# Optimization experiments

Measured on AMD Instinct MI355X. Metric: run time of the kernel, lower is better.

The kernel has to match this reference:

```python
import jax, jax.numpy as jnp
import numpy as np

N_USER = 100000
N_ITEM = 100000
N_EDGE = 1600000
IN_U = 128
IN_I = 128
OUT = 64
NEG_SLOPE = 0.01  # torch F.leaky_relu default


def setup_inputs() -> dict:
    key = jax.random.key(0)
    ks = jax.random.split(key, 12)
    return {
        'feat_user': jax.random.normal(ks[0], (N_USER, IN_U), jnp.float32),
        'feat_item': jax.random.normal(ks[1], (N_ITEM, IN_I), jnp.float32),
        'W_user': jax.random.normal(ks[2], (IN_U, OUT), jnp.float32) * 0.05,
        'b_user': jax.random.normal(ks[3], (OUT,), jnp.float32) * 0.05,
        'W_item': jax.random.normal(ks[4], (IN_I, OUT), jnp.float32) * 0.05,
        'b_item': jax.random.normal(ks[5], (OUT,), jnp.float32) * 0.05,
        'attn_w': jax.random.normal(ks[6], (2 * OUT, 1), jnp.float32) * 0.05,
        'src_u2i': jax.random.randint(ks[7], (N_EDGE,), 0, N_USER),
        'dst_u2i': jax.random.randint(ks[8], (N_EDGE,), 0, N_ITEM),
        'src_i2u': jax.random.randint(ks[9], (N_EDGE,), 0, N_ITEM),
        'dst_i2u': jax.random.randint(ks[10], (N_EDGE,), 0, N_USER),
    }


def _segment_softmax(e, seg, num_segments):
    # e: [E], seg: [E] destination ids -> softmax over edges sharing a dst
    m = jax.ops.segment_max(e, seg, num_segments=num_segments)
    ex = jnp.exp(e - m[seg])
    s = jax.ops.segment_sum(ex, seg, num_segments=num_segments)
    return ex / s[seg]


def _etype_aggregate(Wh_src, Wh_dst, attn_w, src, dst, n_dst):
    # gather per-edge src/dst projected features: [E, OUT]
    zs = Wh_src[src]
    zd = Wh_dst[dst]
    # attn([zs || zd]) == zs @ a_src + zd @ a_dst (split the 2*OUT weight)
    a_src, a_dst = attn_w[:OUT, 0], attn_w[OUT:, 0]
    e = zs @ a_src + zd @ a_dst  # [E]
    e = jnp.where(e > 0, e, NEG_SLOPE * e)  # leaky_relu
    alpha = _segment_softmax(e, dst, n_dst)  # [E]
    # weighted scatter-sum into destination nodes
    return jax.ops.segment_sum(alpha[:, None] * zs, dst, num_segments=n_dst)


def reference(feat_user, feat_item, W_user, b_user, W_item, b_item, attn_w,
              src_u2i, dst_u2i, src_i2u, dst_i2u):
    Wh_user = feat_user @ W_user + b_user  # fc['user'] (etype 'user': user->item)
    Wh_item = feat_item @ W_item + b_item  # fc['item'] (etype 'item': item->user)
    # etype 'user': user -> item; dst attention feature is Wh_item on item nodes
    h_item = _etype_aggregate(Wh_user, Wh_item, attn_w, src_u2i, dst_u2i, N_ITEM)
    # etype 'item': item -> user
    h_user = _etype_aggregate(Wh_item, Wh_user, attn_w, src_i2u, dst_i2u, N_USER)
    # update_nodes sums all 'self_*' per ntype; each ntype has exactly one here
    return jnp.concatenate([h_user, h_item], axis=0)  # [N_USER+N_ITEM, OUT]
```

## Files before the change

### kernel.cpp

```cpp
#include <hip/hip_runtime.h>
#include <hip/hip_bf16.h>

#define NU 100000
#define NI 100000
#define NE 1600000
#define KIN 128
#define KOUT 64

#define NCOPY 8
#define PBK 128
#define NP 782
#define CAP2 384
#define CHUNK 4096
#define SRTSZ (NCOPY * CAP2 + PBK * 3)
#define AGG_THREADS 512
#define NWAVE 8

__device__ __forceinline__ unsigned short f2bf(float f) {
    unsigned u = __float_as_uint(f);
    unsigned r = (u + 0x7fffu + ((u >> 16) & 1u)) >> 16;
    return (unsigned short)r;
}
__device__ __forceinline__ float bf2f(unsigned short h) {
    return __uint_as_float(((unsigned)h) << 16);
}

__global__ __launch_bounds__(256) void linear_attn_kernel(
    const float* __restrict__ A0, const float* __restrict__ W0, const float* __restrict__ bv0,
    const float* __restrict__ A1, const float* __restrict__ W1, const float* __restrict__ bv1,
    const float* __restrict__ attn,
    unsigned short* __restrict__ Wh0, float* __restrict__ su0, float* __restrict__ sd0,
    unsigned short* __restrict__ Wh1, float* __restrict__ su1, float* __restrict__ sd1)
{
    __shared__ float4 Wl[128 * 16];
    __shared__ float  Al[16 * 132];
    __shared__ float  bl[64];
    __shared__ float  asrc[64], adst[64];

    int half = gridDim.x >> 1;
    bool second = blockIdx.x >= (unsigned)half;
    const float* A = second ? A1 : A0;
    const float* W = second ? W1 : W0;
    const float* bvec = second ? bv1 : bv0;
    unsigned short* Wh = second ? Wh1 : Wh0;
    float* s_src = second ? su1 : su0;
    float* s_dst = second ? sd1 : sd0;
    int blk = second ? (blockIdx.x - half) : blockIdx.x;

    int t = threadIdx.x;
    for (int i = t; i < 128 * 16; i += 256) Wl[i] = ((const float4*)W)[i];
    if (t < 64) { bl[t] = bvec[t]; asrc[t] = attn[t]; adst[t] = attn[64 + t]; }
    __syncthreads();

    int r  = t >> 4;
    int k4 = t & 15;
    int nChunks = NU / 16;
    for (int c = blk; c < nChunks; c += half) {
        const float4* Ag = (const float4*)(A + (size_t)c * 16 * 128);
        __syncthreads();
        for (int i = t; i < 512; i += 256) {
            float4 v = Ag[i];
            int rr = i >> 5;
            int cc = (i & 31) * 4;
            float* dp = &Al[rr * 132 + cc];
            dp[0] = v.x; dp[1] = v.y; dp[2] = v.z; dp[3] = v.w;
        }
        __syncthreads();

        float4 acc = {0.f, 0.f, 0.f, 0.f};
        const float* arow = &Al[r * 132];
        #pragma unroll 8
        for (int kk = 0; kk < 128; kk++) {
            float a = arow[kk];
            float4 w = Wl[kk * 16 + k4];
            acc.x += a * w.x; acc.y += a * w.y; acc.z += a * w.z; acc.w += a * w.w;
        }
        acc.x += bl[k4 * 4 + 0]; acc.y += bl[k4 * 4 + 1];
        acc.z += bl[k4 * 4 + 2]; acc.w += bl[k4 * 4 + 3];

        int row = c * 16 + r;
        ushort4 o;
        o.x = f2bf(acc.x); o.y = f2bf(acc.y); o.z = f2bf(acc.z); o.w = f2bf(acc.w);
        ((ushort4*)(Wh + (size_t)row * KOUT))[k4] = o;

        float p1 = acc.x * asrc[k4*4] + acc.y * asrc[k4*4+1] + acc.z * asrc[k4*4+2] + acc.w * asrc[k4*4+3];
        float p2 = acc.x * adst[k4*4] + acc.y * adst[k4*4+1] + acc.z * adst[k4*4+2] + acc.w * adst[k4*4+3];
        #pragma unroll
        for (int off = 8; off; off >>= 1) {
            p1 += __shfl_down(p1, off);
            p2 += __shfl_down(p2, off);
        }
        if (k4 == 0) { s_src[row] = p1; s_dst[row] = p2; }
    }
}

__global__ __launch_bounds__(256) void scatter_kernel(
    const int* __restrict__ src_u2i, const int* __restrict__ dst_u2i,
    const int* __restrict__ src_i2u, const int* __restrict__ dst_i2u,
    int* __restrict__ cur_item, int* __restrict__ cur_user,
    int* __restrict__ ebuf_item, int* __restrict__ ebuf_user,
    int nE, int nbs)
{
    __shared__ int raw[CHUNK];
    __shared__ unsigned short bkt[CHUNK];
    __shared__ int cnt[NP];
    __shared__ int gbase[NP];
    __shared__ int lcur[NP];

    bool u2i = blockIdx.x < (unsigned)nbs;
    int blk = u2i ? blockIdx.x : (blockIdx.x - nbs);
    int copy = blockIdx.x & (NCOPY - 1);
    const int* src = u2i ? src_u2i : src_i2u;
    const int* dst = u2i ? dst_u2i : dst_i2u;
    int* cur  = (u2i ? cur_item : cur_user) + copy * NP;
    int* ebuf = (u2i ? ebuf_item : ebuf_user) + (size_t)copy * NP * CAP2;

    int t = threadIdx.x;
    for (int i = t; i < NP; i += 256) { cnt[i] = 0; lcur[i] = 0; }
    __syncthreads();

    int e0 = blk * CHUNK;
    int n = nE - e0; if (n > CHUNK) n = CHUNK;

    for (int j = t; j < n; j += 256) {
        int s = src[e0 + j], d = dst[e0 + j];
        int b = d >> 7;
        raw[j] = s | ((d & 127) << 17);
        bkt[j] = (unsigned short)b;
        atomicAdd(&cnt[b], 1);
    }
    __syncthreads();

    for (int b = t; b < NP; b += 256) {
        int c = cnt[b];
        if (c) gbase[b] = atomicAdd(&cur[b], c);
    }
    __syncthreads();

    for (int j = t; j < n; j += 256) {
        int b = bkt[j];
        int p = gbase[b] + atomicAdd(&lcur[b], 1);
        if (p < CAP2) ebuf[(size_t)b * CAP2 + p] = raw[j];
    }
}

__global__ __launch_bounds__(AGG_THREADS) void agg_kernel(
    const int* __restrict__ cur_item, const int* __restrict__ cur_user,
    const int* __restrict__ ebuf_item, const int* __restrict__ ebuf_user,
    const float* __restrict__ su_user, const float* __restrict__ sd_item,
    const float* __restrict__ su_item, const float* __restrict__ sd_user,
    const unsigned short* __restrict__ Wh_user, const unsigned short* __restrict__ Wh_item,
    float* __restrict__ h_item, float* __restrict__ h_user)
{
    __shared__ int   raw[SRTSZ];
    __shared__ int   srt[SRTSZ];
    __shared__ int   offs[NCOPY + 1];
    __shared__ int   cnt[PBK];
    __shared__ int   base[PBK + 1];
    __shared__ int   cursor[PBK];
    __shared__ float sdl[PBK];

    int bid = blockIdx.x;
    bool item_side = bid < NP;
    int b = item_side ? bid : bid - NP;
    const int*   cur  = item_side ? cur_item : cur_user;
    const int*   ebuf = item_side ? ebuf_item : ebuf_user;
    const float* ssrc = item_side ? su_user : su_item;
    const float* sdst = item_side ? sd_item : sd_user;
    const unsigned short* Whs = item_side ? Wh_user : Wh_item;
    float* h = item_side ? h_item : h_user;

    int t = threadIdx.x;
    if (t < PBK) {
        cnt[t] = 0;
        int node = b * PBK + t;
        sdl[t] = (node < NU) ? sdst[node] : 0.f;
    }
    if (t == 0) {
        int a = 0;
        #pragma unroll
        for (int c = 0; c < NCOPY; c++) {
            offs[c] = a;
            int cc = cur[c * NP + b];
            if (cc > CAP2) cc = CAP2;
            a += cc;
        }
        offs[NCOPY] = a;
    }
    for (int j = t; j < SRTSZ; j += AGG_THREADS) srt[j] = 0;
    __syncthreads();

    int total = offs[NCOPY];

    for (int j = t; j < total; j += AGG_THREADS) {
        int c = 0;
        while (j >= offs[c + 1]) c++;
        int e = ebuf[((size_t)c * NP + b) * CAP2 + (j - offs[c])];
        raw[j] = e;
        atomicAdd(&cnt[e >> 17], 1);
    }
    __syncthreads();

    if (t == 0) {
        int a = 0;
        for (int i = 0; i < PBK; i++) {
            base[i] = a; cursor[i] = a;
            a += (cnt[i] + 3) & ~3;
        }
        base[PBK] = a;
    }
    __syncthreads();

    for (int j = t; j < total; j += AGG_THREADS) {
        int e = raw[j];
        int p = atomicAdd(&cursor[e >> 17], 1);
        srt[p] = e;
    }
    __syncthreads();

    int lane = t & 63;
    int wv = t >> 6;

    float* wgt = (float*)raw;
    for (int dl = wv; dl < PBK; dl += NWAVE) {
        int jb = base[dl], cc = cnt[dl], pc = base[dl + 1] - jb;
        float sd = sdl[dl];
        for (int k = lane; k < pc; k += 64) {
            float w = 0.f;
            if (k < cc) {
                int s = srt[jb + k] & 0x1FFFF;
                float ev = ssrc[s] + sd;
                ev = ev > 0.f ? ev : 0.01f * ev;
                w = __expf(ev);
            }
            wgt[jb + k] = w;
        }
    }
    __syncthreads();

    int sub = lane >> 4;
    int ch4 = (lane & 15) << 2;
    const unsigned short* WhCh = Whs + ch4;
    for (int dl = wv; dl < PBK; dl += NWAVE) {
        int node = b * PBK + dl;
        if (node >= NU) break;
        int jb = base[dl];
        int pc = base[dl + 1] - jb;
        int cc = cnt[dl];
        float ax = 0.f, ay = 0.f, az = 0.f, aw = 0.f, ssum = 0.f;
        for (int q = 0; q < pc; q += 4) {
            int j = jb + q + sub;
            int e = srt[j];
            float w = wgt[j];
            int s = e & 0x1FFFF;
            uint2 u = *(const uint2*)(WhCh + ((size_t)s << 6));
            float f0 = __uint_as_float(u.x << 16);
            float f1 = __uint_as_float(u.x & 0xffff0000u);
            float f2 = __uint_as_float(u.y << 16);
            float f3 = __uint_as_float(u.y & 0xffff0000u);
            ax += w * f0; ay += w * f1; az += w * f2; aw += w * f3;
            ssum += w;
        }
        #pragma unroll
        for (int off = 16; off <= 32; off <<= 1) {
            ax += __shfl_xor(ax, off);
            ay += __shfl_xor(ay, off);
            az += __shfl_xor(az, off);
            aw += __shfl_xor(aw, off);
            ssum += __shfl_xor(ssum, off);
        }
        if (sub == 0) {
            float inv = (cc > 0) ? 1.f / ssum : 0.f;
            float4 o = {ax * inv, ay * inv, az * inv, aw * inv};
            *(float4*)(h + (size_t)node * KOUT + ch4) = o;
        }
    }
}

extern "C" void kernel_launch(void* const* d_in, const int* in_sizes, int n_in,
                              void* d_out, int out_size, void* d_ws, size_t ws_size,
                              hipStream_t stream)
{
    const float* feat_user = (const float*)d_in[0];
    const float* feat_item = (const float*)d_in[1];
    const float* W_user    = (const float*)d_in[2];
    const float* b_user    = (const float*)d_in[3];
    const float* W_item    = (const float*)d_in[4];
    const float* b_item    = (const float*)d_in[5];
    const float* attn_w    = (const float*)d_in[6];
    const int*   src_u2i   = (const int*)d_in[7];
    const int*   dst_u2i   = (const int*)d_in[8];
    const int*   src_i2u   = (const int*)d_in[9];
    const int*   dst_i2u   = (const int*)d_in[10];

    float* out    = (float*)d_out;
    float* h_user = out;
    float* h_item = out + (size_t)NU * KOUT;

    char* p = (char*)d_ws;
    unsigned short* Wh_user = (unsigned short*)p; p += (size_t)NU * KOUT * 2;
    unsigned short* Wh_item = (unsigned short*)p; p += (size_t)NI * KOUT * 2;
    float* su_user = (float*)p; p += NU * 4;
    float* sd_user = (float*)p; p += NU * 4;
    float* su_item = (float*)p; p += NI * 4;
    float* sd_item = (float*)p; p += NI * 4;
    int* cur_item  = (int*)p; p += (size_t)NCOPY * NP * 4;
    int* cur_user  = (int*)p; p += (size_t)NCOPY * NP * 4;
    int* ebuf_item = (int*)p; p += (size_t)NCOPY * NP * CAP2 * 4;
    int* ebuf_user = (int*)p; p += (size_t)NCOPY * NP * CAP2 * 4;

    hipMemsetAsync(cur_item, 0, (size_t)2 * NCOPY * NP * 4, stream);

    int nbs = (NE + CHUNK - 1) / CHUNK;
    scatter_kernel<<<2 * nbs, 256, 0, stream>>>(src_u2i, dst_u2i, src_i2u, dst_i2u,
                                                cur_item, cur_user, ebuf_item, ebuf_user,
                                                NE, nbs);
    linear_attn_kernel<<<4096, 256, 0, stream>>>(feat_user, W_user, b_user,
                                                 feat_item, W_item, b_item, attn_w,
                                                 Wh_user, su_user, sd_user,
                                                 Wh_item, su_item, sd_item);
    agg_kernel<<<2 * NP, AGG_THREADS, 0, stream>>>(cur_item, cur_user, ebuf_item, ebuf_user,
                                                   su_user, sd_item, su_item, sd_user,
                                                   Wh_user, Wh_item, h_item, h_user);
}
```

Before: 356.2 us.

## Register-tile the projection GEMM and locally sort edges before global scatter

The linear projection kernel now gives each thread a 4x4 output micro-tile over a 64-row shared tile, using float4 loads of A and W, with a smaller persistent grid. This raises arithmetic intensity per shared-memory read. The scatter kernel now counting-sorts each chunk by destination bucket in shared memory before writing to global buffers, so writes to each bucket are contiguous. In exchange it uses more shared memory and adds an extra prefix-scan pass and barrier.

```diff
diff --git a/kernel.cpp b/kernel.cpp
--- a/kernel.cpp
+++ b/kernel.cpp
@@ -16,6 +16,10 @@
 #define AGG_THREADS 512
 #define NWAVE 8
 
+#define LIN_ROWS 64
+#define LIN_GRID 512
+#define LIN_ITERS 1563
+
 __device__ __forceinline__ unsigned short f2bf(float f) {
     unsigned u = __float_as_uint(f);
     unsigned r = (u + 0x7fffu + ((u >> 16) & 1u)) >> 16;
@@ -32,10 +36,8 @@
     unsigned short* __restrict__ Wh0, float* __restrict__ su0, float* __restrict__ sd0,
     unsigned short* __restrict__ Wh1, float* __restrict__ su1, float* __restrict__ sd1)
 {
-    __shared__ float4 Wl[128 * 16];
-    __shared__ float  Al[16 * 132];
-    __shared__ float  bl[64];
-    __shared__ float  asrc[64], adst[64];
+    __shared__ float Wl[128 * 64];
+    __shared__ float Al[LIN_ROWS * 132];
 
     int half = gridDim.x >> 1;
     bool second = blockIdx.x >= (unsigned)half;
@@ -48,49 +50,78 @@
     int blk = second ? (blockIdx.x - half) : blockIdx.x;
 
     int t = threadIdx.x;
-    for (int i = t; i < 128 * 16; i += 256) Wl[i] = ((const float4*)W)[i];
-    if (t < 64) { bl[t] = bvec[t]; asrc[t] = attn[t]; adst[t] = attn[64 + t]; }
-    __syncthreads();
-
-    int r  = t >> 4;
-    int k4 = t & 15;
-    int nChunks = NU / 16;
-    for (int c = blk; c < nChunks; c += half) {
-        const float4* Ag = (const float4*)(A + (size_t)c * 16 * 128);
+    int c4 = t & 15;
+    int rt = t >> 4;
+
+    for (int i = t; i < 128 * 64 / 4; i += 256) ((float4*)Wl)[i] = ((const float4*)W)[i];
+
+    float4 bias4 = *(const float4*)(bvec + c4 * 4);
+    float4 as4   = *(const float4*)(attn + c4 * 4);
+    float4 ad4   = *(const float4*)(attn + 64 + c4 * 4);
+
+    for (int c = blk; c < LIN_ITERS; c += half) {
+        int rowbase = c * LIN_ROWS;
         __syncthreads();
-        for (int i = t; i < 512; i += 256) {
-            float4 v = Ag[i];
-            int rr = i >> 5;
-            int cc = (i & 31) * 4;
-            float* dp = &Al[rr * 132 + cc];
-            dp[0] = v.x; dp[1] = v.y; dp[2] = v.z; dp[3] = v.w;
+        for (int g = t; g < LIN_ROWS * 32; g += 256) {
+            int rr = g >> 5;
+            int q  = g & 31;
+            float4 v = {0.f, 0.f, 0.f, 0.f};
+            int grow = rowbase + rr;
+            if (grow < NU) v = ((const float4*)(A + (size_t)grow * 128))[q];
+            *(float4*)&Al[rr * 132 + q * 4] = v;
         }
         __syncthreads();
 
-        float4 acc = {0.f, 0.f, 0.f, 0.f};
-        const float* arow = &Al[r * 132];
-        #pragma unroll 8
-        for (int kk = 0; kk < 128; kk++) {
-            float a = arow[kk];
-            float4 w = Wl[kk * 16 + k4];
-            acc.x += a * w.x; acc.y += a * w.y; acc.z += a * w.z; acc.w += a * w.w;
-        }
-        acc.x += bl[k4 * 4 + 0]; acc.y += bl[k4 * 4 + 1];
-        acc.z += bl[k4 * 4 + 2]; acc.w += bl[k4 * 4 + 3];
-
-        int row = c * 16 + r;
-        ushort4 o;
-        o.x = f2bf(acc.x); o.y = f2bf(acc.y); o.z = f2bf(acc.z); o.w = f2bf(acc.w);
-        ((ushort4*)(Wh + (size_t)row * KOUT))[k4] = o;
-
-        float p1 = acc.x * asrc[k4*4] + acc.y * asrc[k4*4+1] + acc.z * asrc[k4*4+2] + acc.w * asrc[k4*4+3];
-        float p2 = acc.x * adst[k4*4] + acc.y * adst[k4*4+1] + acc.z * adst[k4*4+2] + acc.w * adst[k4*4+3];
+        float4 acc0 = bias4, acc1 = bias4, acc2 = bias4, acc3 = bias4;
+        const float* Ar = &Al[(rt * 4) * 132];
+        const float* Wc = &Wl[c4 * 4];
+        #pragma unroll 4
+        for (int kq = 0; kq < 128; kq += 4) {
+            float4 a0 = *(const float4*)&Ar[0 * 132 + kq];
+            float4 a1 = *(const float4*)&Ar[1 * 132 + kq];
+            float4 a2 = *(const float4*)&Ar[2 * 132 + kq];
+            float4 a3 = *(const float4*)&Ar[3 * 132 + kq];
+            float4 w0 = *(const float4*)&Wc[(kq + 0) * 64];
+            float4 w1 = *(const float4*)&Wc[(kq + 1) * 64];
+            float4 w2 = *(const float4*)&Wc[(kq + 2) * 64];
+            float4 w3 = *(const float4*)&Wc[(kq + 3) * 64];
+            acc0.x += a0.x*w0.x + a0.y*w1.x + a0.z*w2.x + a0.w*w3.x;
+            acc0.y += a0.x*w0.y + a0.y*w1.y + a0.z*w2.y + a0.w*w3.y;
+            acc0.z += a0.x*w0.z + a0.y*w1.z + a0.z*w2.z + a0.w*w3.z;
+            acc0.w += a0.x*w0.w + a0.y*w1.w + a0.z*w2.w + a0.w*w3.w;
+            acc1.x += a1.x*w0.x + a1.y*w1.x + a1.z*w2.x + a1.w*w3.x;
+            acc1.y += a1.x*w0.y + a1.y*w1.y + a1.z*w2.y + a1.w*w3.y;
+            acc1.z += a1.x*w0.z + a1.y*w1.z + a1.z*w2.z + a1.w*w3.z;
+            acc1.w += a1.x*w0.w + a1.y*w1.w + a1.z*w2.w + a1.w*w3.w;
+            acc2.x += a2.x*w0.x + a2.y*w1.x + a2.z*w2.x + a2.w*w3.x;
+            acc2.y += a2.x*w0.y + a2.y*w1.y + a2.z*w2.y + a2.w*w3.y;
+            acc2.z += a2.x*w0.z + a2.y*w1.z + a2.z*w2.z + a2.w*w3.z;
+            acc2.w += a2.x*w0.w + a2.y*w1.w + a2.z*w2.w + a2.w*w3.w;
+            acc3.x += a3.x*w0.x + a3.y*w1.x + a3.z*w2.x + a3.w*w3.x;
+            acc3.y += a3.x*w0.y + a3.y*w1.y + a3.z*w2.y + a3.w*w3.y;
+            acc3.z += a3.x*w0.z + a3.y*w1.z + a3.z*w2.z + a3.w*w3.z;
+            acc3.w += a3.x*w0.w + a3.y*w1.w + a3.z*w2.w + a3.w*w3.w;
+        }
+
+        float4 accs[4] = {acc0, acc1, acc2, acc3};
         #pragma unroll
-        for (int off = 8; off; off >>= 1) {
-            p1 += __shfl_down(p1, off);
-            p2 += __shfl_down(p2, off);
-        }
-        if (k4 == 0) { s_src[row] = p1; s_dst[row] = p2; }
+        for (int i = 0; i < 4; i++) {
+            int row = rowbase + rt * 4 + i;
+            float4 av = accs[i];
+            if (row < NU) {
+                ushort4 o;
+                o.x = f2bf(av.x); o.y = f2bf(av.y); o.z = f2bf(av.z); o.w = f2bf(av.w);
+                ((ushort4*)(Wh + (size_t)row * KOUT))[c4] = o;
+            }
+            float p1 = av.x*as4.x + av.y*as4.y + av.z*as4.z + av.w*as4.w;
+            float p2 = av.x*ad4.x + av.y*ad4.y + av.z*ad4.z + av.w*ad4.w;
+            #pragma unroll
+            for (int off = 8; off; off >>= 1) {
+                p1 += __shfl_down(p1, off, 16);
+                p2 += __shfl_down(p2, off, 16);
+            }
+            if (c4 == 0 && row < NU) { s_src[row] = p1; s_dst[row] = p2; }
+        }
     }
 }
 
@@ -103,9 +134,12 @@
 {
     __shared__ int raw[CHUNK];
     __shared__ unsigned short bkt[CHUNK];
+    __shared__ int srt_[CHUNK];
+    __shared__ unsigned short sbk[CHUNK];
     __shared__ int cnt[NP];
-    __shared__ int gbase[NP];
-    __shared__ int lcur[NP];
+    __shared__ int gb[NP];
+    __shared__ int pb[NP];
+    __shared__ int lc[NP];
 
     bool u2i = blockIdx.x < (unsigned)nbs;
     int blk = u2i ? blockIdx.x : (blockIdx.x - nbs);
@@ -116,7 +150,7 @@
     int* ebuf = (u2i ? ebuf_item : ebuf_user) + (size_t)copy * NP * CAP2;
 
     int t = threadIdx.x;
-    for (int i = t; i < NP; i += 256) { cnt[i] = 0; lcur[i] = 0; }
+    for (int i = t; i < NP; i += 256) cnt[i] = 0;
     __syncthreads();
 
     int e0 = blk * CHUNK;
@@ -133,14 +167,39 @@
 
     for (int b = t; b < NP; b += 256) {
         int c = cnt[b];
-        if (c) gbase[b] = atomicAdd(&cur[b], c);
+        gb[b] = c ? atomicAdd(&cur[b], c) : 0;
+    }
+    if (t < 64) {
+        int lo = t * 13;
+        int hi = lo + 13; if (hi > NP) hi = NP; if (lo > NP) lo = NP;
+        int s = 0;
+        for (int i = lo; i < hi; i++) s += cnt[i];
+        int run = s;
+        #pragma unroll
+        for (int off = 1; off < 64; off <<= 1) {
+            int v = __shfl_up(run, off);
+            if (t >= off) run += v;
+        }
+        int excl = run - s;
+        for (int i = lo; i < hi; i++) {
+            pb[i] = excl; lc[i] = excl;
+            excl += cnt[i];
+        }
     }
     __syncthreads();
 
     for (int j = t; j < n; j += 256) {
         int b = bkt[j];
-        int p = gbase[b] + atomicAdd(&lcur[b], 1);
-        if (p < CAP2) ebuf[(size_t)b * CAP2 + p] = raw[j];
+        int p = atomicAdd(&lc[b], 1);
+        srt_[p] = raw[j];
+        sbk[p] = (unsigned short)b;
+    }
+    __syncthreads();
+
+    for (int j = t; j < n; j += 256) {
+        int b = sbk[j];
+        int pos = gb[b] + (j - pb[b]);
+        if (pos < CAP2) ebuf[(size_t)b * CAP2 + pos] = srt_[j];
     }
 }
 
@@ -315,10 +374,10 @@
     scatter_kernel<<<2 * nbs, 256, 0, stream>>>(src_u2i, dst_u2i, src_i2u, dst_i2u,
                                                 cur_item, cur_user, ebuf_item, ebuf_user,
                                                 NE, nbs);
-    linear_attn_kernel<<<4096, 256, 0, stream>>>(feat_user, W_user, b_user,
-                                                 feat_item, W_item, b_item, attn_w,
-                                                 Wh_user, su_user, sd_user,
-                                                 Wh_item, su_item, sd_item);
+    linear_attn_kernel<<<LIN_GRID, 256, 0, stream>>>(feat_user, W_user, b_user,
+                                                     feat_item, W_item, b_item, attn_w,
+                                                     Wh_user, su_user, sd_user,
+                                                     Wh_item, su_item, sd_item);
     agg_kernel<<<2 * NP, AGG_THREADS, 0, stream>>>(cur_item, cur_user, ebuf_item, ebuf_user,
                                                    su_user, sd_item, su_item, sd_user,
                                                    Wh_user, Wh_item, h_item, h_user);
```

Result: no change. 358.9 us (+0.8%).
